# Performance work log

Hardware: AMD Instinct MI355X
Metric: run time of the kernel (lower is better)

## Reference

```python
import jax, jax.numpy as jnp
import numpy as np

DIM = 256   # model dim (forced by gate Linear(32,4): d = 32 = DIM//H)
H = 8       # heads (hard-coded by mask.repeat(1,8,1,1))
D = DIM // H
B = 256     # batch
NS = 100    # skeleton tokens (sub-block size)
NQ = 64     # query tokens
N = NS + NQ # 164
NE = 4      # experts
HID = 50    # expert hidden
LN_EPS = 1e-5


def setup_inputs() -> dict:
    key = jax.random.key(0)
    ks = jax.random.split(key, 12)
    s = 0.02
    return {
        "x": jax.random.normal(ks[0], (B, N, DIM), jnp.float32),
        "mask": jax.random.randint(ks[1], (B, N), 0, 2).astype(bool),
        "w_qk_s": jax.random.normal(ks[2], (DIM, 2 * DIM), jnp.float32) * s,
        "w_qk_q": jax.random.normal(ks[3], (DIM, 2 * DIM), jnp.float32) * s,
        "w_v": jax.random.normal(ks[4], (DIM, DIM), jnp.float32) * s,
        "w_gate": jax.random.normal(ks[5], (D, NE), jnp.float32) * s,
        "b_gate": jnp.zeros((NE,), jnp.float32),
        "ln_gamma": jnp.ones((NE,), jnp.float32),
        "ln_beta": jnp.zeros((NE,), jnp.float32),
        "w1": jax.random.normal(ks[6], (NE, NS, HID), jnp.float32) * s,
        "b1": jnp.zeros((NE, HID), jnp.float32),
        "w2": jax.random.normal(ks[7], (NE, HID, NS), jnp.float32) * s,
        "b2": jnp.zeros((NE, NS), jnp.float32),
        "w_out": jax.random.normal(ks[8], (DIM, DIM), jnp.float32) * s,
        "b_out": jnp.zeros((DIM,), jnp.float32),
    }


def reference(x, mask, w_qk_s, w_qk_q, w_v, w_gate, b_gate, ln_gamma, ln_beta,
              w1, b1, w2, b2, w_out, b_out):
    b, n, dim = x.shape
    scale = dim ** -0.5  # scale_with_head=False -> dim**-0.5

    def to_heads(t):  # (b, m, H*D) -> (b, H, m, D)
        return t.reshape(b, -1, H, D).transpose(0, 2, 1, 3)

    # separate qk projections for skeleton (first 100) vs query (last 64) tokens
    q_s, k_s = jnp.split(x[:, :NS] @ w_qk_s, 2, axis=-1)
    q_q, k_q = jnp.split(x[:, NS:] @ w_qk_q, 2, axis=-1)
    q = jnp.concatenate([to_heads(q_s), to_heads(q_q)], axis=2)  # (b,H,N,D)
    k = jnp.concatenate([to_heads(k_s), to_heads(k_q)], axis=2)
    v = to_heads(x @ w_v)

    # gates: RAW reshape of x (b,n,H*D) -> (b,H,n,D) (memory reinterpretation,
    # as in torch x.reshape), detached, sliced to first 100 'rows'
    gx = jax.lax.stop_gradient(x).reshape(b, H, n, D)[:, :, :NS, :]
    g = gx @ w_gate + b_gate                              # (b,H,100,4)
    mu = g.mean(-1, keepdims=True)
    var = g.var(-1, keepdims=True)
    g = (g - mu) / jnp.sqrt(var + LN_EPS) * ln_gamma + ln_beta
    gates = jax.nn.softmax(g, axis=-1)                    # (b,H,100,4)

    dots = jnp.einsum('bhid,bhjd->bhij', q, k) * scale    # (b,H,N,N)
    mask_value = -jnp.finfo(dots.dtype).max
    dots = jnp.where(mask[:, None, None, :], mask_value, dots)

    # soft-MoE over the 100x100 sub-block (experts applied along key axis)
    attn_q = dots[:, :, :NS, :NS]                         # (b,H,100,100)
    h1 = jax.nn.relu(jnp.einsum('bhij,ejk->bheik', jax.nn.relu(attn_q), w1)
                     + b1[:, None, :])                    # (b,H,4,100,50)
    eo = jax.nn.relu(jnp.einsum('bheik,ekj->bheij', h1, w2)
                     + b2[:, None, :])                    # (b,H,4,100,100)
    moes = jnp.einsum('bheij,bhie->bhij', eo, gates)      # (b,H,100,100)

    dots = dots.at[:, :, :NS, :NS].add(moes)
    attn = jax.nn.softmax(dots, axis=-1)
    out = jnp.einsum('bhij,bhjd->bhid', attn, v)          # (b,H,N,D)
    out = out.transpose(0, 2, 1, 3).reshape(b, n, dim)
    return out @ w_out + b_out
```

## Files before the change

kernel.cpp:

```cpp
#include <hip/hip_runtime.h>

typedef __bf16 bf16x8 __attribute__((ext_vector_type(8)));
typedef float  f32x4  __attribute__((ext_vector_type(4)));

__device__ __forceinline__ bf16x8 ldb8(const __bf16* p) {
    return *reinterpret_cast<const bf16x8*>(p);
}
__device__ __forceinline__ bf16x8 zero8() {
    bf16x8 z;
    #pragma unroll
    for (int i = 0; i < 8; i++) z[i] = (__bf16)0.f;
    return z;
}
__device__ __forceinline__ __bf16 ldw(const void* p, int i, int m) {
    return m ? (__bf16)((const float*)p)[i] : ((const __bf16*)p)[i];
}
__device__ __forceinline__ bf16x8 ldx8(const void* p, size_t ei, int m) {
    if (m) {
        const float* f = (const float*)p + ei;
        f32x4 a = *reinterpret_cast<const f32x4*>(f);
        f32x4 b = *reinterpret_cast<const f32x4*>(f + 4);
        bf16x8 r;
        #pragma unroll
        for (int u = 0; u < 4; u++) { r[u] = (__bf16)a[u]; r[4 + u] = (__bf16)b[u]; }
        return r;
    }
    return ldb8((const __bf16*)p + ei);
}

__global__ __launch_bounds__(256) void detect_kernel(
    const void* x, const void* mask, int* modes, int* maskws)
{
    __shared__ int sbad, v32bad, v16bad;
    const int t = threadIdx.x;
    if (t == 0) { sbad = 0; v32bad = 0; v16bad = 0; }
    __syncthreads();
    const unsigned int* xw = (const unsigned int*)x;
    int bad = 0;
    for (int i = t; i < 2048; i += 256) {
        unsigned int w = xw[i];
        unsigned int el = (w >> 7) & 0xFF, eh = (w >> 23) & 0xFF;
        if (el >= 0x94 || el == 0xFF) bad++;
        if (eh >= 0x94 || eh == 0xFF) bad++;
    }
    if (bad) atomicAdd(&sbad, bad);
    const unsigned int* mw = (const unsigned int*)mask;
    int b32 = 0, b16 = 0;
    for (int i = t; i < 10496; i += 256) {
        unsigned int w = mw[i];
        if (!(w == 0u || w == 1u || w == 0x3F800000u)) b32++;
        unsigned int h0 = w & 0xFFFFu, h1 = w >> 16;
        if (!(h0 == 0u || h0 == 1u || h0 == 0x3F80u)) b16++;
        if (!(h1 == 0u || h1 == 1u || h1 == 0x3F80u)) b16++;
    }
    if (b32) atomicAdd(&v32bad, b32);
    if (b16) atomicAdd(&v16bad, b16);
    __syncthreads();
    const int mode_x = (sbad > 64) ? 1 : 0;
    const int mmode = (v32bad == 0) ? 0 : ((v16bad == 0) ? 2 : 1);
    if (t == 0) { modes[0] = mode_x; modes[1] = mmode; }
    for (int i = t; i < 41984; i += 256) {
        int val;
        if (mmode == 0)      val = (((const int*)mask)[i] != 0);
        else if (mmode == 2) val = (((const unsigned short*)mask)[i] != 0);
        else                 val = (((const unsigned char*)mask)[i] != 0);
        maskws[i] = val;
    }
}

__global__ __launch_bounds__(256) void prep_kernel(
    const void* wqks, const void* wqkq, const void* wv, const void* w1,
    const void* w2, const void* wout, const void* wg, const void* bg,
    const void* lng, const void* lnb, const void* b1, const void* b2,
    const void* bout, const int* __restrict__ modes,
    __bf16* __restrict__ Wts, __bf16* __restrict__ Wtq,
    __bf16* __restrict__ w1t, __bf16* __restrict__ w2t,
    __bf16* __restrict__ wot, __bf16* __restrict__ wsm)
{
    const int m = modes[0];
    int i = blockIdx.x * 256 + threadIdx.x;
    if (i < 196608) {
        int n = i >> 8, k = i & 255;
        __bf16 vs, vq;
        if (n < 512) { vs = ldw(wqks, k * 512 + n, m); vq = ldw(wqkq, k * 512 + n, m); }
        else         { vs = ldw(wv, k * 256 + (n - 512), m); vq = vs; }
        Wts[i] = vs; Wtq[i] = vq;
        return;
    }
    i -= 196608;
    if (i < 32768) {
        int e = i >> 13, r = i & 8191, n = r >> 7, k = r & 127;
        w1t[i] = (n < 50 && k < 100) ? ldw(w1, (e * 100 + k) * 50 + n, m) : (__bf16)0.f;
        return;
    }
    i -= 32768;
    if (i < 28672) {
        int e = i / 7168, r = i % 7168, n = r >> 6, k = r & 63;
        w2t[i] = (n < 100 && k < 50) ? ldw(w2, (e * 50 + k) * 100 + n, m) : (__bf16)0.f;
        return;
    }
    i -= 28672;
    if (i < 65536) {
        int n = i >> 8, k = i & 255;
        wot[i] = ldw(wout, k * 256 + n, m);
        return;
    }
    i -= 65536;
    if (i < 996) {
        __bf16 v;
        if (i < 128)      v = ldw(wg, i, m);
        else if (i < 132) v = ldw(bg, i - 128, m);
        else if (i < 136) v = ldw(lng, i - 132, m);
        else if (i < 140) v = ldw(lnb, i - 136, m);
        else if (i < 340) v = ldw(b1, i - 140, m);
        else if (i < 740) v = ldw(b2, i - 340, m);
        else              v = ldw(bout, i - 740, m);
        wsm[i] = v;
    }
}

__global__ __launch_bounds__(128) void gate_kernel(
    const void* __restrict__ x, const __bf16* __restrict__ wsm,
    const int* __restrict__ modes, float* __restrict__ gates)
{
    __shared__ float wgs[128];
    __shared__ float bgs[4], gs[4], bs[4];
    const int bh = blockIdx.x, t = threadIdx.x;
    wgs[t] = (float)wsm[t];
    if (t < 4) { bgs[t] = (float)wsm[128 + t]; gs[t] = (float)wsm[132 + t]; bs[t] = (float)wsm[136 + t]; }
    __syncthreads();
    if (t >= 100) return;
    const int m = modes[0];
    const int b = bh >> 3, h = bh & 7;
    const size_t base = (size_t)b * 41984 + h * 5248 + t * 32;
    float g[4] = {bgs[0], bgs[1], bgs[2], bgs[3]};
    #pragma unroll
    for (int p = 0; p < 4; p++) {
        bf16x8 xv = ldx8(x, base + p * 8, m);
        #pragma unroll
        for (int u = 0; u < 8; u++) {
            float f = (float)xv[u];
            #pragma unroll
            for (int e = 0; e < 4; e++) g[e] += f * wgs[(p * 8 + u) * 4 + e];
        }
    }
    float mu = 0.25f * (g[0] + g[1] + g[2] + g[3]);
    float var = 0.25f * ((g[0]-mu)*(g[0]-mu) + (g[1]-mu)*(g[1]-mu) +
                         (g[2]-mu)*(g[2]-mu) + (g[3]-mu)*(g[3]-mu));
    float is = rsqrtf(var + 1e-5f);
    float mx = -3.0e38f;
    #pragma unroll
    for (int e = 0; e < 4; e++) { g[e] = (g[e] - mu) * is * gs[e] + bs[e]; mx = fmaxf(mx, g[e]); }
    float s = 0.f;
    #pragma unroll
    for (int e = 0; e < 4; e++) { g[e] = __expf(g[e] - mx); s += g[e]; }
    float inv = 1.f / s;
    float* gp = gates + ((size_t)bh * 100 + t) * 4;
    #pragma unroll
    for (int e = 0; e < 4; e++) gp[e] = g[e] * inv;
}

__global__ __launch_bounds__(256, 2) void qkv_kernel(
    const void* __restrict__ x, const __bf16* __restrict__ Wts,
    const __bf16* __restrict__ Wtq, const int* __restrict__ modes,
    __bf16* __restrict__ q, __bf16* __restrict__ k, __bf16* __restrict__ v)
{
    __shared__ __bf16 xs[32][264];
    const int m = modes[0];
    const int b = blockIdx.y;
    const int mt = blockIdx.x;
    const __bf16* Wt = (mt < 4) ? Wts : Wtq;
    const int rbase = (mt < 4) ? mt * 32 : 100 + (mt - 4) * 32;
    const int tid = threadIdx.x;

    for (int c = tid; c < 1024; c += 256) {
        int row = c >> 5, part = c & 31;
        bf16x8 val = ldx8(x, ((size_t)b * 164 + rbase + row) * 256 + part * 8, m);
        *reinterpret_cast<bf16x8*>(&xs[row][part * 8]) = val;
    }
    __syncthreads();

    const int w = tid >> 6, l = tid & 63, lr = l & 15, lc = l >> 4;
    f32x4 acc[2][12];
    #pragma unroll
    for (int ms = 0; ms < 2; ms++)
        #pragma unroll
        for (int nt = 0; nt < 12; nt++) acc[ms][nt] = (f32x4){0.f, 0.f, 0.f, 0.f};

    #pragma unroll
    for (int kt = 0; kt < 8; kt++) {
        bf16x8 a0 = ldb8(&xs[lr][kt * 32 + lc * 8]);
        bf16x8 a1 = ldb8(&xs[16 + lr][kt * 32 + lc * 8]);
        #pragma unroll
        for (int nt = 0; nt < 12; nt++) {
            bf16x8 bb = ldb8(Wt + (size_t)(w * 192 + nt * 16 + lr) * 256 + kt * 32 + lc * 8);
            acc[0][nt] = __builtin_amdgcn_mfma_f32_16x16x32_bf16(a0, bb, acc[0][nt], 0, 0, 0);
            acc[1][nt] = __builtin_amdgcn_mfma_f32_16x16x32_bf16(a1, bb, acc[1][nt], 0, 0, 0);
        }
    }
    #pragma unroll
    for (int ms = 0; ms < 2; ms++) {
        #pragma unroll
        for (int nt = 0; nt < 12; nt++) {
            int c = w * 192 + nt * 16 + lr;
            __bf16* dst; int ch;
            if (c < 256)      { dst = q; ch = c; }
            else if (c < 512) { dst = k; ch = c - 256; }
            else              { dst = v; ch = c - 512; }
            int hh = ch >> 5, d = ch & 31;
            #pragma unroll
            for (int r = 0; r < 4; r++) {
                int i = rbase + ms * 16 + lc * 4 + r;
                if (mt >= 4 || i < 100)
                    dst[(((size_t)b * 8 + hh) * 164 + i) * 32 + d] = (__bf16)acc[ms][nt][r];
            }
        }
    }
}

__global__ __launch_bounds__(256, 3) void attn_kernel(
    const __bf16* __restrict__ qg, const __bf16* __restrict__ kg,
    const __bf16* __restrict__ vg, const float* __restrict__ gatesg,
    const int* __restrict__ maskg, const __bf16* __restrict__ w1t,
    const __bf16* __restrict__ w2t, const __bf16* __restrict__ wsm,
    __bf16* __restrict__ ohg)
{
    __shared__ __bf16 KV[7680];
    __shared__ __bf16 S[64][200];
    __shared__ __bf16 h1s[64][72];
    __shared__ float  gtile[64][4];
    __shared__ int    kmask[192];

    const __bf16* b1g = wsm + 140;
    const __bf16* b2g = wsm + 340;
    const int bh = blockIdx.x, rt = blockIdx.y, b = bh >> 3, tid = threadIdx.x;

    const __bf16* kbase = kg + (size_t)bh * 164 * 32;
    for (int c = tid; c < 768; c += 256) {
        int row = c >> 2, part = c & 3;
        bf16x8 val = (row < 164) ? ldb8(kbase + row * 32 + part * 8) : zero8();
        *reinterpret_cast<bf16x8*>(&KV[row * 40 + part * 8]) = val;
    }
    for (int j = tid; j < 192; j += 256)
        kmask[j] = (j < 164) ? maskg[b * 164 + j] : 1;
    {
        int il = tid >> 2, e = tid & 3, gi = rt * 64 + il;
        gtile[il][e] = (gi < 100) ? gatesg[((size_t)bh * 100 + gi) * 4 + e] : 0.f;
    }
    __syncthreads();

    const int w = tid >> 6, l = tid & 63, lr = l & 15, lc = l >> 4;
    const int m0 = w * 16;

    int qrow = rt * 64 + m0 + lr; if (qrow > 163) qrow = 163;
    bf16x8 afq = ldb8(qg + ((size_t)bh * 164 + qrow) * 32 + lc * 8);
    f32x4 raw[12];
    #pragma unroll
    for (int nt = 0; nt < 12; nt++) {
        bf16x8 bf = ldb8(&KV[(nt * 16 + lr) * 40 + lc * 8]);
        f32x4 acc = {0.f, 0.f, 0.f, 0.f};
        acc = __builtin_amdgcn_mfma_f32_16x16x32_bf16(afq, bf, acc, 0, 0, 0);
        int j = nt * 16 + lr;
        bool bad = (kmask[j] != 0);
        #pragma unroll
        for (int r = 0; r < 4; r++)
            raw[nt][r] = bad ? -1e30f : acc[r] * 0.0625f;
    }
    #pragma unroll
    for (int nt = 0; nt < 8; nt++) {
        int j = nt * 16 + lr;
        #pragma unroll
        for (int r = 0; r < 4; r++) {
            float v = raw[nt][r];
            v = (j >= 100 || v < 0.f) ? 0.f : v;
            S[m0 + lc * 4 + r][j] = (__bf16)v;
        }
    }
    __syncthreads();

    const __bf16* vbase = vg + (size_t)bh * 164 * 32;
    for (int c = tid; c < 656; c += 256) {
        int j = c >> 2, part = c & 3;
        bf16x8 val = ldb8(vbase + j * 32 + part * 8);
        #pragma unroll
        for (int u = 0; u < 8; u++) KV[(part * 8 + u) * 200 + j] = val[u];
    }
    for (int c = tid; c < 896; c += 256) {
        int d = c & 31, j = 164 + (c >> 5);
        KV[d * 200 + j] = (__bf16)0.f;
    }

    if (rt < 2) {
        for (int e = 0; e < 4; e++) {
            #pragma unroll
            for (int nt = 0; nt < 4; nt++) {
                f32x4 acc = {0.f, 0.f, 0.f, 0.f};
                #pragma unroll
                for (int kt = 0; kt < 4; kt++) {
                    bf16x8 sa = ldb8(&S[m0 + lr][kt * 32 + lc * 8]);
                    bf16x8 bb = ldb8(w1t + (size_t)(e * 64 + nt * 16 + lr) * 128 + kt * 32 + lc * 8);
                    acc = __builtin_amdgcn_mfma_f32_16x16x32_bf16(sa, bb, acc, 0, 0, 0);
                }
                int n = nt * 16 + lr;
                float bias = (n < 50) ? (float)b1g[e * 50 + n] : 0.f;
                #pragma unroll
                for (int r = 0; r < 4; r++) {
                    float v = acc[r] + bias;
                    if (v < 0.f) v = 0.f;
                    h1s[m0 + lc * 4 + r][n] = (__bf16)v;
                }
            }
            bf16x8 ha0 = ldb8(&h1s[m0 + lr][lc * 8]);
            bf16x8 ha1 = ldb8(&h1s[m0 + lr][32 + lc * 8]);
            float gt[4];
            #pragma unroll
            for (int r = 0; r < 4; r++) gt[r] = gtile[m0 + lc * 4 + r][e];
            #pragma unroll
            for (int nt = 0; nt < 7; nt++) {
                f32x4 acc = {0.f, 0.f, 0.f, 0.f};
                bf16x8 bb0 = ldb8(w2t + (size_t)(e * 112 + nt * 16 + lr) * 64 + lc * 8);
                acc = __builtin_amdgcn_mfma_f32_16x16x32_bf16(ha0, bb0, acc, 0, 0, 0);
                bf16x8 bb1 = ldb8(w2t + (size_t)(e * 112 + nt * 16 + lr) * 64 + 32 + lc * 8);
                acc = __builtin_amdgcn_mfma_f32_16x16x32_bf16(ha1, bb1, acc, 0, 0, 0);
                int n = nt * 16 + lr;
                float bias = (n < 100) ? (float)b2g[e * 100 + n] : 0.f;
                #pragma unroll
                for (int r = 0; r < 4; r++) {
                    float v = acc[r] + bias;
                    if (v < 0.f) v = 0.f;
                    raw[nt][r] += v * gt[r];
                }
            }
        }
    }

    #pragma unroll
    for (int r = 0; r < 4; r++) {
        float m2 = -3.0e38f;
        #pragma unroll
        for (int nt = 0; nt < 12; nt++) m2 = fmaxf(m2, raw[nt][r]);
        m2 = fmaxf(m2, __shfl_xor(m2, 1, 64));
        m2 = fmaxf(m2, __shfl_xor(m2, 2, 64));
        m2 = fmaxf(m2, __shfl_xor(m2, 4, 64));
        m2 = fmaxf(m2, __shfl_xor(m2, 8, 64));
        float s2 = 0.f;
        #pragma unroll
        for (int nt = 0; nt < 12; nt++) {
            float ev = __expf(raw[nt][r] - m2);
            raw[nt][r] = ev;
            s2 += ev;
        }
        s2 += __shfl_xor(s2, 1, 64);
        s2 += __shfl_xor(s2, 2, 64);
        s2 += __shfl_xor(s2, 4, 64);
        s2 += __shfl_xor(s2, 8, 64);
        float inv = (s2 > 0.f) ? 1.f / s2 : 0.f;
        #pragma unroll
        for (int nt = 0; nt < 12; nt++)
            S[m0 + lc * 4 + r][nt * 16 + lr] = (__bf16)(raw[nt][r] * inv);
    }
    __syncthreads();

    #pragma unroll
    for (int nt = 0; nt < 2; nt++) {
        f32x4 acc = {0.f, 0.f, 0.f, 0.f};
        #pragma unroll
        for (int kt = 0; kt < 6; kt++) {
            bf16x8 pa = ldb8(&S[m0 + lr][kt * 32 + lc * 8]);
            bf16x8 bb = ldb8(&KV[(nt * 16 + lr) * 200 + kt * 32 + lc * 8]);
            acc = __builtin_amdgcn_mfma_f32_16x16x32_bf16(pa, bb, acc, 0, 0, 0);
        }
        int d = nt * 16 + lr;
        #pragma unroll
        for (int r = 0; r < 4; r++) {
            int gi = rt * 64 + m0 + lc * 4 + r;
            if (gi < 164)
                ohg[((size_t)bh * 164 + gi) * 32 + d] = (__bf16)acc[r];
        }
    }
}

__global__ __launch_bounds__(256) void outproj_kernel(
    const __bf16* __restrict__ oh, const __bf16* __restrict__ wot,
    const __bf16* __restrict__ wsm, float* __restrict__ out)
{
    const __bf16* bout = wsm + 740;
    const int b = blockIdx.y;
    const int mt = blockIdx.x >> 1;
    const int ntile = blockIdx.x & 1;
    const int tid = threadIdx.x;
    const int w = tid >> 6, l = tid & 63, lr = l & 15, lc = l >> 4;
    int row = mt * 64 + w * 16 + lr; if (row > 163) row = 163;
    f32x4 acc[8];
    #pragma unroll
    for (int nt = 0; nt < 8; nt++) acc[nt] = (f32x4){0.f, 0.f, 0.f, 0.f};
    #pragma unroll
    for (int kt = 0; kt < 8; kt++) {
        bf16x8 a = ldb8(oh + (((size_t)b * 8 + kt) * 164 + row) * 32 + lc * 8);
        #pragma unroll
        for (int nt = 0; nt < 8; nt++) {
            bf16x8 bb = ldb8(wot + (size_t)(ntile * 128 + nt * 16 + lr) * 256 + kt * 32 + lc * 8);
            acc[nt] = __builtin_amdgcn_mfma_f32_16x16x32_bf16(a, bb, acc[nt], 0, 0, 0);
        }
    }
    #pragma unroll
    for (int nt = 0; nt < 8; nt++) {
        int n = ntile * 128 + nt * 16 + lr;
        float bias = (float)bout[n];
        #pragma unroll
        for (int r = 0; r < 4; r++) {
            int i = mt * 64 + w * 16 + lc * 4 + r;
            if (i < 164)
                out[((size_t)b * 164 + i) * 256 + n] = acc[nt][r] + bias;
        }
    }
}

extern "C" void kernel_launch(void* const* d_in, const int* in_sizes, int n_in,
                              void* d_out, int out_size, void* d_ws, size_t ws_size,
                              hipStream_t stream) {
    const void* x      = d_in[0];
    const void* mask   = d_in[1];
    const void* w_qk_s = d_in[2];
    const void* w_qk_q = d_in[3];
    const void* w_v    = d_in[4];
    const void* w_gate = d_in[5];
    const void* b_gate = d_in[6];
    const void* ln_g   = d_in[7];
    const void* ln_b   = d_in[8];
    const void* w1     = d_in[9];
    const void* b1     = d_in[10];
    const void* w2     = d_in[11];
    const void* b2     = d_in[12];
    const void* w_out  = d_in[13];
    const void* b_out  = d_in[14];
    float* out = (float*)d_out;

    char* ws = (char*)d_ws;
    size_t off = 0;
    auto nextp = [&](size_t bytes) {
        char* p = ws + off;
        off += (bytes + 255) & ~(size_t)255;
        return p;
    };
    const size_t QKV_ELEMS = (size_t)256 * 8 * 164 * 32;
    int*    modes  = (int*)nextp(64);
    int*    maskws = (int*)nextp((size_t)41984 * 4);
    __bf16* qws  = (__bf16*)nextp(QKV_ELEMS * 2);
    __bf16* kws  = (__bf16*)nextp(QKV_ELEMS * 2);
    __bf16* vws  = (__bf16*)nextp(QKV_ELEMS * 2);
    __bf16* ohws = (__bf16*)nextp(QKV_ELEMS * 2);
    float*  gws  = (float*)nextp((size_t)2048 * 100 * 4 * 4);
    __bf16* Wts  = (__bf16*)nextp(768 * 256 * 2);
    __bf16* Wtq  = (__bf16*)nextp(768 * 256 * 2);
    __bf16* w1t  = (__bf16*)nextp(4 * 64 * 128 * 2);
    __bf16* w2t  = (__bf16*)nextp(4 * 112 * 64 * 2);
    __bf16* wot  = (__bf16*)nextp(256 * 256 * 2);
    __bf16* wsm  = (__bf16*)nextp(996 * 2);

    detect_kernel<<<1, 256, 0, stream>>>(x, mask, modes, maskws);
    prep_kernel<<<1268, 256, 0, stream>>>(w_qk_s, w_qk_q, w_v, w1, w2, w_out,
                                          w_gate, b_gate, ln_g, ln_b, b1, b2,
                                          b_out, modes, Wts, Wtq, w1t, w2t, wot, wsm);
    gate_kernel<<<2048, 128, 0, stream>>>(x, wsm, modes, gws);
    qkv_kernel<<<dim3(6, 256), 256, 0, stream>>>(x, Wts, Wtq, modes, qws, kws, vws);
    attn_kernel<<<dim3(2048, 3), 256, 0, stream>>>(qws, kws, vws, gws, maskws,
                                                   w1t, w2t, wsm, ohws);
    outproj_kernel<<<dim3(6, 256), 256, 0, stream>>>(ohws, wot, wsm, out);
}
```

Before: 601.6 us.

## Fuse gate into QKV kernel, parallelize detect, and shrink attention LDS footprint

Removes the separate gate kernel by computing the gate LayerNorm+softmax from the x tile already staged in shared memory inside the QKV kernel, saving a launch and a re-read of x. The detect/mask-conversion kernel now runs on 64 blocks instead of one. The attention kernel packs its shared buffers into one aliased region, keeps the key mask as per-lane bits in a register, drops the fully padded key tile, and raises the occupancy hint to 4 blocks per CU. It also transposes V with a gather layout, reads gates straight from global memory, and writes output vectorized by swapping the MFMA operands. The trade-offs are an extra barrier, aliasing hazards between the score, probability and V regions, and more scattered global loads for V and gates.

Measured after the change: 554.7 us. 1.08x faster.

```diff
diff --git a/kernel.cpp b/kernel.cpp
--- a/kernel.cpp
+++ b/kernel.cpp
@@ -1,6 +1,7 @@
 #include <hip/hip_runtime.h>
 
 typedef __bf16 bf16x8 __attribute__((ext_vector_type(8)));
+typedef __bf16 bf16x4 __attribute__((ext_vector_type(4)));
 typedef float  f32x4  __attribute__((ext_vector_type(4)));
 
 __device__ __forceinline__ bf16x8 ldb8(const __bf16* p) {
@@ -31,19 +32,10 @@
 __global__ __launch_bounds__(256) void detect_kernel(
     const void* x, const void* mask, int* modes, int* maskws)
 {
-    __shared__ int sbad, v32bad, v16bad;
-    const int t = threadIdx.x;
-    if (t == 0) { sbad = 0; v32bad = 0; v16bad = 0; }
-    __syncthreads();
-    const unsigned int* xw = (const unsigned int*)x;
-    int bad = 0;
-    for (int i = t; i < 2048; i += 256) {
-        unsigned int w = xw[i];
-        unsigned int el = (w >> 7) & 0xFF, eh = (w >> 23) & 0xFF;
-        if (el >= 0x94 || el == 0xFF) bad++;
-        if (eh >= 0x94 || eh == 0xFF) bad++;
-    }
-    if (bad) atomicAdd(&sbad, bad);
+    __shared__ int v32bad, v16bad, sbad;
+    const int t = threadIdx.x, bid = blockIdx.x;
+    if (t == 0) { v32bad = 0; v16bad = 0; sbad = 0; }
+    __syncthreads();
     const unsigned int* mw = (const unsigned int*)mask;
     int b32 = 0, b16 = 0;
     for (int i = t; i < 10496; i += 256) {
@@ -55,11 +47,22 @@
     }
     if (b32) atomicAdd(&v32bad, b32);
     if (b16) atomicAdd(&v16bad, b16);
-    __syncthreads();
-    const int mode_x = (sbad > 64) ? 1 : 0;
+    if (bid == 0) {
+        const unsigned int* xw = (const unsigned int*)x;
+        int bad = 0;
+        for (int i = t; i < 2048; i += 256) {
+            unsigned int w = xw[i];
+            unsigned int el = (w >> 7) & 0xFF, eh = (w >> 23) & 0xFF;
+            if (el >= 0x94 || el == 0xFF) bad++;
+            if (eh >= 0x94 || eh == 0xFF) bad++;
+        }
+        if (bad) atomicAdd(&sbad, bad);
+    }
+    __syncthreads();
     const int mmode = (v32bad == 0) ? 0 : ((v16bad == 0) ? 2 : 1);
-    if (t == 0) { modes[0] = mode_x; modes[1] = mmode; }
-    for (int i = t; i < 41984; i += 256) {
+    if (bid == 0 && t == 0) { modes[0] = (sbad > 64) ? 1 : 0; modes[1] = mmode; }
+    const int lo = bid * 656, hi = lo + 656;
+    for (int i = lo + t; i < hi; i += 256) {
         int val;
         if (mmode == 0)      val = (((const int*)mask)[i] != 0);
         else if (mmode == 2) val = (((const unsigned short*)mask)[i] != 0);
@@ -119,53 +122,16 @@
     }
 }
 
-__global__ __launch_bounds__(128) void gate_kernel(
-    const void* __restrict__ x, const __bf16* __restrict__ wsm,
-    const int* __restrict__ modes, float* __restrict__ gates)
-{
-    __shared__ float wgs[128];
-    __shared__ float bgs[4], gs[4], bs[4];
-    const int bh = blockIdx.x, t = threadIdx.x;
-    wgs[t] = (float)wsm[t];
-    if (t < 4) { bgs[t] = (float)wsm[128 + t]; gs[t] = (float)wsm[132 + t]; bs[t] = (float)wsm[136 + t]; }
-    __syncthreads();
-    if (t >= 100) return;
-    const int m = modes[0];
-    const int b = bh >> 3, h = bh & 7;
-    const size_t base = (size_t)b * 41984 + h * 5248 + t * 32;
-    float g[4] = {bgs[0], bgs[1], bgs[2], bgs[3]};
-    #pragma unroll
-    for (int p = 0; p < 4; p++) {
-        bf16x8 xv = ldx8(x, base + p * 8, m);
-        #pragma unroll
-        for (int u = 0; u < 8; u++) {
-            float f = (float)xv[u];
-            #pragma unroll
-            for (int e = 0; e < 4; e++) g[e] += f * wgs[(p * 8 + u) * 4 + e];
-        }
-    }
-    float mu = 0.25f * (g[0] + g[1] + g[2] + g[3]);
-    float var = 0.25f * ((g[0]-mu)*(g[0]-mu) + (g[1]-mu)*(g[1]-mu) +
-                         (g[2]-mu)*(g[2]-mu) + (g[3]-mu)*(g[3]-mu));
-    float is = rsqrtf(var + 1e-5f);
-    float mx = -3.0e38f;
-    #pragma unroll
-    for (int e = 0; e < 4; e++) { g[e] = (g[e] - mu) * is * gs[e] + bs[e]; mx = fmaxf(mx, g[e]); }
-    float s = 0.f;
-    #pragma unroll
-    for (int e = 0; e < 4; e++) { g[e] = __expf(g[e] - mx); s += g[e]; }
-    float inv = 1.f / s;
-    float* gp = gates + ((size_t)bh * 100 + t) * 4;
-    #pragma unroll
-    for (int e = 0; e < 4; e++) gp[e] = g[e] * inv;
-}
-
 __global__ __launch_bounds__(256, 2) void qkv_kernel(
     const void* __restrict__ x, const __bf16* __restrict__ Wts,
-    const __bf16* __restrict__ Wtq, const int* __restrict__ modes,
-    __bf16* __restrict__ q, __bf16* __restrict__ k, __bf16* __restrict__ v)
+    const __bf16* __restrict__ Wtq, const __bf16* __restrict__ wsm,
+    const int* __restrict__ modes,
+    __bf16* __restrict__ q, __bf16* __restrict__ k, __bf16* __restrict__ v,
+    float* __restrict__ gates)
 {
     __shared__ __bf16 xs[32][264];
+    __shared__ float wgf[128];
+    __shared__ float gcst[12];
     const int m = modes[0];
     const int b = blockIdx.y;
     const int mt = blockIdx.x;
@@ -173,12 +139,50 @@
     const int rbase = (mt < 4) ? mt * 32 : 100 + (mt - 4) * 32;
     const int tid = threadIdx.x;
 
+    if (tid < 128) wgf[tid] = (float)wsm[tid];
+    if (tid < 12)  gcst[tid] = (float)wsm[128 + tid];
     for (int c = tid; c < 1024; c += 256) {
         int row = c >> 5, part = c & 31;
         bf16x8 val = ldx8(x, ((size_t)b * 164 + rbase + row) * 256 + part * 8, m);
         *reinterpret_cast<bf16x8*>(&xs[row][part * 8]) = val;
     }
     __syncthreads();
+
+    {
+        int jg = rbase * 8 + tid;
+        int h = jg / 164;
+        int j = jg - h * 164;
+        if (j < 100) {
+            const __bf16* xp = &xs[tid >> 3][(tid & 7) * 32];
+            float g[4] = {gcst[0], gcst[1], gcst[2], gcst[3]};
+            #pragma unroll
+            for (int p = 0; p < 4; p++) {
+                bf16x8 xv = ldb8(xp + p * 8);
+                #pragma unroll
+                for (int u = 0; u < 8; u++) {
+                    float f = (float)xv[u];
+                    #pragma unroll
+                    for (int e = 0; e < 4; e++) g[e] += f * wgf[(p * 8 + u) * 4 + e];
+                }
+            }
+            float mu = 0.25f * (g[0] + g[1] + g[2] + g[3]);
+            float var = 0.25f * ((g[0]-mu)*(g[0]-mu) + (g[1]-mu)*(g[1]-mu) +
+                                 (g[2]-mu)*(g[2]-mu) + (g[3]-mu)*(g[3]-mu));
+            float is = rsqrtf(var + 1e-5f);
+            float mx = -3.0e38f;
+            #pragma unroll
+            for (int e = 0; e < 4; e++) {
+                g[e] = (g[e] - mu) * is * gcst[4 + e] + gcst[8 + e];
+                mx = fmaxf(mx, g[e]);
+            }
+            float s = 0.f;
+            #pragma unroll
+            for (int e = 0; e < 4; e++) { g[e] = __expf(g[e] - mx); s += g[e]; }
+            float inv = 1.f / s;
+            float4 gv = make_float4(g[0]*inv, g[1]*inv, g[2]*inv, g[3]*inv);
+            *reinterpret_cast<float4*>(&gates[((size_t)(b * 8 + h) * 100 + j) * 4]) = gv;
+        }
+    }
 
     const int w = tid >> 6, l = tid & 63, lr = l & 15, lc = l >> 4;
     f32x4 acc[2][12];
@@ -218,54 +222,55 @@
     }
 }
 
-__global__ __launch_bounds__(256, 3) void attn_kernel(
+__global__ __launch_bounds__(256, 4) void attn_kernel(
     const __bf16* __restrict__ qg, const __bf16* __restrict__ kg,
     const __bf16* __restrict__ vg, const float* __restrict__ gatesg,
     const int* __restrict__ maskg, const __bf16* __restrict__ w1t,
     const __bf16* __restrict__ w2t, const __bf16* __restrict__ wsm,
     __bf16* __restrict__ ohg)
 {
-    __shared__ __bf16 KV[7680];
-    __shared__ __bf16 S[64][200];
-    __shared__ __bf16 h1s[64][72];
-    __shared__ float  gtile[64][4];
-    __shared__ int    kmask[192];
+    __shared__ __align__(16) __bf16 lds[20352];
+    const int RS_OFF = 7040;
+    const int H1_OFF = 15744;
+    const int P_OFF  = 7040;
 
     const __bf16* b1g = wsm + 140;
     const __bf16* b2g = wsm + 340;
     const int bh = blockIdx.x, rt = blockIdx.y, b = bh >> 3, tid = threadIdx.x;
+    const int w = tid >> 6, l = tid & 63, lr = l & 15, lc = l >> 4;
+    const int m0 = w * 16;
 
     const __bf16* kbase = kg + (size_t)bh * 164 * 32;
-    for (int c = tid; c < 768; c += 256) {
+    for (int c = tid; c < 704; c += 256) {
         int row = c >> 2, part = c & 3;
         bf16x8 val = (row < 164) ? ldb8(kbase + row * 32 + part * 8) : zero8();
-        *reinterpret_cast<bf16x8*>(&KV[row * 40 + part * 8]) = val;
-    }
-    for (int j = tid; j < 192; j += 256)
-        kmask[j] = (j < 164) ? maskg[b * 164 + j] : 1;
-    {
-        int il = tid >> 2, e = tid & 3, gi = rt * 64 + il;
-        gtile[il][e] = (gi < 100) ? gatesg[((size_t)bh * 100 + gi) * 4 + e] : 0.f;
-    }
-    __syncthreads();
-
-    const int w = tid >> 6, l = tid & 63, lr = l & 15, lc = l >> 4;
-    const int m0 = w * 16;
+        *reinterpret_cast<bf16x8*>(&lds[row * 40 + part * 8]) = val;
+    }
+    unsigned mbits = 0;
+    #pragma unroll
+    for (int nt = 0; nt < 11; nt++) {
+        int j = nt * 16 + lr;
+        int bad = (j < 164) ? maskg[b * 164 + j] : 1;
+        mbits |= (bad ? 1u : 0u) << nt;
+    }
+    __syncthreads();
 
     int qrow = rt * 64 + m0 + lr; if (qrow > 163) qrow = 163;
     bf16x8 afq = ldb8(qg + ((size_t)bh * 164 + qrow) * 32 + lc * 8);
     f32x4 raw[12];
     #pragma unroll
-    for (int nt = 0; nt < 12; nt++) {
-        bf16x8 bf = ldb8(&KV[(nt * 16 + lr) * 40 + lc * 8]);
+    for (int nt = 0; nt < 11; nt++) {
+        bf16x8 bf = ldb8(&lds[(nt * 16 + lr) * 40 + lc * 8]);
         f32x4 acc = {0.f, 0.f, 0.f, 0.f};
         acc = __builtin_amdgcn_mfma_f32_16x16x32_bf16(afq, bf, acc, 0, 0, 0);
-        int j = nt * 16 + lr;
-        bool bad = (kmask[j] != 0);
+        bool bad = (mbits >> nt) & 1;
         #pragma unroll
         for (int r = 0; r < 4; r++)
             raw[nt][r] = bad ? -1e30f : acc[r] * 0.0625f;
     }
+    #pragma unroll
+    for (int r = 0; r < 4; r++) raw[11][r] = -1e30f;
+
     #pragma unroll
     for (int nt = 0; nt < 8; nt++) {
         int j = nt * 16 + lr;
@@ -273,33 +278,42 @@
         for (int r = 0; r < 4; r++) {
             float v = raw[nt][r];
             v = (j >= 100 || v < 0.f) ? 0.f : v;
-            S[m0 + lc * 4 + r][j] = (__bf16)v;
+            lds[RS_OFF + (m0 + lc * 4 + r) * 136 + j] = (__bf16)v;
         }
     }
     __syncthreads();
 
     const __bf16* vbase = vg + (size_t)bh * 164 * 32;
-    for (int c = tid; c < 656; c += 256) {
-        int j = c >> 2, part = c & 3;
-        bf16x8 val = ldb8(vbase + j * 32 + part * 8);
-        #pragma unroll
-        for (int u = 0; u < 8; u++) KV[(part * 8 + u) * 200 + j] = val[u];
-    }
-    for (int c = tid; c < 896; c += 256) {
-        int d = c & 31, j = 164 + (c >> 5);
-        KV[d * 200 + j] = (__bf16)0.f;
+    {
+        int dd = tid & 31;
+        #pragma unroll
+        for (int p = 0; p < 3; p++) {
+            int jg = (tid >> 5) + p * 8;
+            int j0 = jg * 8;
+            bf16x8 vv = zero8();
+            if (j0 < 164) {
+                #pragma unroll
+                for (int u = 0; u < 8; u++)
+                    if (j0 + u < 164) vv[u] = vbase[(size_t)(j0 + u) * 32 + dd];
+            }
+            *reinterpret_cast<bf16x8*>(&lds[dd * 200 + j0]) = vv;
+        }
     }
 
     if (rt < 2) {
+        const int gi0 = rt * 64 + m0 + lc * 4;
         for (int e = 0; e < 4; e++) {
+            bf16x8 sa[4];
+            #pragma unroll
+            for (int kt = 0; kt < 4; kt++)
+                sa[kt] = ldb8(&lds[RS_OFF + (m0 + lr) * 136 + kt * 32 + lc * 8]);
             #pragma unroll
             for (int nt = 0; nt < 4; nt++) {
                 f32x4 acc = {0.f, 0.f, 0.f, 0.f};
                 #pragma unroll
                 for (int kt = 0; kt < 4; kt++) {
-                    bf16x8 sa = ldb8(&S[m0 + lr][kt * 32 + lc * 8]);
                     bf16x8 bb = ldb8(w1t + (size_t)(e * 64 + nt * 16 + lr) * 128 + kt * 32 + lc * 8);
-                    acc = __builtin_amdgcn_mfma_f32_16x16x32_bf16(sa, bb, acc, 0, 0, 0);
+                    acc = __builtin_amdgcn_mfma_f32_16x16x32_bf16(sa[kt], bb, acc, 0, 0, 0);
                 }
                 int n = nt * 16 + lr;
                 float bias = (n < 50) ? (float)b1g[e * 50 + n] : 0.f;
@@ -307,14 +321,17 @@
                 for (int r = 0; r < 4; r++) {
                     float v = acc[r] + bias;
                     if (v < 0.f) v = 0.f;
-                    h1s[m0 + lc * 4 + r][n] = (__bf16)v;
+                    lds[H1_OFF + (m0 + lc * 4 + r) * 72 + n] = (__bf16)v;
                 }
             }
-            bf16x8 ha0 = ldb8(&h1s[m0 + lr][lc * 8]);
-            bf16x8 ha1 = ldb8(&h1s[m0 + lr][32 + lc * 8]);
+            bf16x8 ha0 = ldb8(&lds[H1_OFF + (m0 + lr) * 72 + lc * 8]);
+            bf16x8 ha1 = ldb8(&lds[H1_OFF + (m0 + lr) * 72 + 32 + lc * 8]);
             float gt[4];
             #pragma unroll
-            for (int r = 0; r < 4; r++) gt[r] = gtile[m0 + lc * 4 + r][e];
+            for (int r = 0; r < 4; r++) {
+                int gi = gi0 + r;
+                gt[r] = (gi < 100) ? gatesg[((size_t)bh * 100 + gi) * 4 + e] : 0.f;
+            }
             #pragma unroll
             for (int nt = 0; nt < 7; nt++) {
                 f32x4 acc = {0.f, 0.f, 0.f, 0.f};
@@ -333,6 +350,7 @@
             }
         }
     }
+    __syncthreads();
 
     #pragma unroll
     for (int r = 0; r < 4; r++) {
@@ -357,25 +375,25 @@
         float inv = (s2 > 0.f) ? 1.f / s2 : 0.f;
         #pragma unroll
         for (int nt = 0; nt < 12; nt++)
-            S[m0 + lc * 4 + r][nt * 16 + lr] = (__bf16)(raw[nt][r] * inv);
-    }
-    __syncthreads();
-
+            lds[P_OFF + (m0 + lc * 4 + r) * 200 + nt * 16 + lr] = (__bf16)(raw[nt][r] * inv);
+    }
+    __syncthreads();
+
+    int gi = rt * 64 + m0 + lr;
     #pragma unroll
     for (int nt = 0; nt < 2; nt++) {
         f32x4 acc = {0.f, 0.f, 0.f, 0.f};
         #pragma unroll
         for (int kt = 0; kt < 6; kt++) {
-            bf16x8 pa = ldb8(&S[m0 + lr][kt * 32 + lc * 8]);
-            bf16x8 bb = ldb8(&KV[(nt * 16 + lr) * 200 + kt * 32 + lc * 8]);
-            acc = __builtin_amdgcn_mfma_f32_16x16x32_bf16(pa, bb, acc, 0, 0, 0);
-        }
-        int d = nt * 16 + lr;
-        #pragma unroll
-        for (int r = 0; r < 4; r++) {
-            int gi = rt * 64 + m0 + lc * 4 + r;
-            if (gi < 164)
-                ohg[((size_t)bh * 164 + gi) * 32 + d] = (__bf16)acc[r];
+            bf16x8 va = ldb8(&lds[(nt * 16 + lr) * 200 + kt * 32 + lc * 8]);
+            bf16x8 pb = ldb8(&lds[P_OFF + (m0 + lr) * 200 + kt * 32 + lc * 8]);
+            acc = __builtin_amdgcn_mfma_f32_16x16x32_bf16(va, pb, acc, 0, 0, 0);
+        }
+        if (gi < 164) {
+            bf16x4 ov;
+            #pragma unroll
+            for (int r = 0; r < 4; r++) ov[r] = (__bf16)acc[r];
+            *reinterpret_cast<bf16x4*>(&ohg[((size_t)bh * 164 + gi) * 32 + nt * 16 + lc * 4]) = ov;
         }
     }
 }
@@ -458,12 +476,12 @@
     __bf16* wot  = (__bf16*)nextp(256 * 256 * 2);
     __bf16* wsm  = (__bf16*)nextp(996 * 2);
 
-    detect_kernel<<<1, 256, 0, stream>>>(x, mask, modes, maskws);
+    detect_kernel<<<64, 256, 0, stream>>>(x, mask, modes, maskws);
     prep_kernel<<<1268, 256, 0, stream>>>(w_qk_s, w_qk_q, w_v, w1, w2, w_out,
                                           w_gate, b_gate, ln_g, ln_b, b1, b2,
                                           b_out, modes, Wts, Wtq, w1t, w2t, wot, wsm);
-    gate_kernel<<<2048, 128, 0, stream>>>(x, wsm, modes, gws);
-    qkv_kernel<<<dim3(6, 256), 256, 0, stream>>>(x, Wts, Wtq, modes, qws, kws, vws);
+    qkv_kernel<<<dim3(6, 256), 256, 0, stream>>>(x, Wts, Wtq, wsm, modes,
+                                                 qws, kws, vws, gws);
     attn_kernel<<<dim3(2048, 3), 256, 0, stream>>>(qws, kws, vws, gws, maskws,
                                                    w1t, w2t, wsm, ohws);
     outproj_kernel<<<dim3(6, 256), 256, 0, stream>>>(ohws, wot, wsm, out);
```
